# Performance work log

Measured on AMD Instinct MI355X. Metric: run time of the kernel, lower is better.

## Reference

```python
import jax, jax.numpy as jnp
import numpy as np

NHEADS = 16
DIM = 1024


def setup_inputs() -> dict:
    key = jax.random.key(0)
    k1, k2, k3 = jax.random.split(key, 3)
    B, S, D = 4, 2048, DIM
    x = jax.random.normal(k1, (B, S, D), dtype=jnp.float32)
    W_qkv = jax.random.normal(k2, (D, 3 * D), dtype=jnp.float32) * (1.0 / np.sqrt(D))
    b_qkv = jax.random.normal(k3, (3 * D,), dtype=jnp.float32) * 0.01
    return {"x": x, "W_qkv": W_qkv, "b_qkv": b_qkv}


def reference(x, W_qkv, b_qkv):
    B, S, D = x.shape
    H = NHEADS
    Dh = D // H
    qkv = x @ W_qkv + b_qkv                      # [B, S, 3D]
    q, k, v = jnp.split(qkv, 3, axis=-1)         # each [B, S, D]
    # [B, S, H, Dh] -> [B, H, S, Dh]
    q = q.reshape(B, S, H, Dh).transpose(0, 2, 1, 3)
    k = k.reshape(B, S, H, Dh).transpose(0, 2, 1, 3)
    v = v.reshape(B, S, H, Dh).transpose(0, 2, 1, 3)
    scale = 1.0 / np.sqrt(Dh).astype(np.float32)
    scores = jnp.einsum('bhqd,bhkd->bhqk', q, k) * scale
    attn = jax.nn.softmax(scores, axis=-1)
    out = jnp.einsum('bhqk,bhkd->bhqd', attn, v)  # [B, H, S, Dh]
    # FAITHFUL to original: raw view [B,H,S,Dh] -> [B, S, H*Dh] (no transpose back)
    return out.reshape(B, S, H * Dh)
```

## Files before the change

### kernel.cpp

```cpp
#include <hip/hip_runtime.h>
#include <hip/hip_bf16.h>
#include <stdint.h>

typedef float          f32x4 __attribute__((ext_vector_type(4)));
typedef short          s16x8 __attribute__((ext_vector_type(8)));
typedef unsigned short u16;
typedef u16            u16x4 __attribute__((ext_vector_type(4)));
typedef u16            u16x8 __attribute__((ext_vector_type(8)));

#define DMODEL 1024
#define NH     16
#define DH     64
#define SEQ    2048
#define BATCH  4
#define NROW   (BATCH*SEQ)
#define N3     (3*DMODEL)

#define KEXP 0.1803368801f

__device__ __forceinline__ u16 f2bf(float f) {
    __hip_bfloat16 h = __float2bfloat16(f);
    u16 u;
    __builtin_memcpy(&u, &h, 2);
    return u;
}

typedef const __attribute__((address_space(1))) void* gas_t;
typedef __attribute__((address_space(3))) void* las_t;
__device__ __forceinline__ void async16(void* lds, const void* g) {
    __builtin_amdgcn_global_load_lds((gas_t)g, (las_t)lds, 16, 0, 0);
}

__device__ __forceinline__ f32x4 mfma16(s16x8 a, s16x8 b, f32x4 c) {
    return __builtin_amdgcn_mfma_f32_16x16x32_bf16(a, b, c, 0, 0, 0);
}

__global__ __launch_bounds__(256)
void cast_x_kernel(const float* __restrict__ in, u16* __restrict__ out, int n8) {
    int i = blockIdx.x * 256 + threadIdx.x;
    if (i >= n8) return;
    const f32x4* p = (const f32x4*)in;
    f32x4 a = p[2*i], b = p[2*i+1];
    u16x8 o;
    o[0]=f2bf(a[0]); o[1]=f2bf(a[1]); o[2]=f2bf(a[2]); o[3]=f2bf(a[3]);
    o[4]=f2bf(b[0]); o[5]=f2bf(b[1]); o[6]=f2bf(b[2]); o[7]=f2bf(b[3]);
    ((u16x8*)out)[i] = o;
}

__global__ __launch_bounds__(256)
void castT_w_kernel(const float* __restrict__ W, u16* __restrict__ Wt) {
    __shared__ u16 T[64][72];
    const int t  = threadIdx.x;
    const int n0 = blockIdx.x * 64;
    const int k0 = blockIdx.y * 64;
    {
        const int c4 = t & 15, rr = t >> 4;
        #pragma unroll
        for (int ri = 0; ri < 4; ++ri) {
            const int r = ri*16 + rr;
            f32x4 v = *(const f32x4*)&W[(size_t)(k0 + r) * N3 + n0 + c4*4];
            #pragma unroll
            for (int e = 0; e < 4; ++e) T[r][c4*4+e] = f2bf(v[e]);
        }
    }
    __syncthreads();
    {
        const int nr = t >> 2, kq = t & 3;
        #pragma unroll
        for (int pp = 0; pp < 2; ++pp) {
            const int kb = kq + pp*4;
            u16x8 o;
            #pragma unroll
            for (int e = 0; e < 8; ++e) o[e] = T[kb*8+e][nr];
            *(u16x8*)&Wt[(size_t)(n0 + nr) * DMODEL + k0 + kb*8] = o;
        }
    }
}

__global__ __launch_bounds__(256)
void qkv_mfma_kernel(const u16* __restrict__ xb, const u16* __restrict__ Wt,
                     const float* __restrict__ bias,
                     u16* __restrict__ Qb, u16* __restrict__ Kb, u16* __restrict__ Vt)
{
    __shared__ u16 As[128*32];
    __shared__ u16 Bs[128*32];

    const int tid  = threadIdx.x;
    const int lane = tid & 63;
    const int w    = tid >> 6;
    const int wm   = w >> 1, wn = w & 1;
    const int n0   = blockIdx.x * 128;
    const int m0   = blockIdx.y * 128;

    const int srow = w*32 + (lane >> 2);
    const int scol = (lane & 3) * 8;
    u16* ad0 = &As[(w*2+0)*512 + lane*8];
    u16* ad1 = &As[(w*2+1)*512 + lane*8];
    u16* bd0 = &Bs[(w*2+0)*512 + lane*8];
    u16* bd1 = &Bs[(w*2+1)*512 + lane*8];
    const u16* ag0 = &xb[(size_t)(m0 + srow)      * DMODEL + scol];
    const u16* ag1 = &xb[(size_t)(m0 + srow + 16) * DMODEL + scol];
    const u16* bg0 = &Wt[(size_t)(n0 + srow)      * DMODEL + scol];
    const u16* bg1 = &Wt[(size_t)(n0 + srow + 16) * DMODEL + scol];

    f32x4 acc[4][4];
    #pragma unroll
    for (int i = 0; i < 4; ++i)
        #pragma unroll
        for (int j = 0; j < 4; ++j)
            acc[i][j] = (f32x4){0.f, 0.f, 0.f, 0.f};

    for (int k0 = 0; k0 < DMODEL; k0 += 32) {
        async16(ad0, ag0 + k0);
        async16(ad1, ag1 + k0);
        async16(bd0, bg0 + k0);
        async16(bd1, bg1 + k0);
        __syncthreads();
        s16x8 af[4], bf[4];
        #pragma unroll
        for (int mi = 0; mi < 4; ++mi)
            af[mi] = *(const s16x8*)&As[(wm*64 + mi*16 + (lane&15))*32 + (lane>>4)*8];
        #pragma unroll
        for (int ni = 0; ni < 4; ++ni)
            bf[ni] = *(const s16x8*)&Bs[(wn*64 + ni*16 + (lane&15))*32 + (lane>>4)*8];
        #pragma unroll
        for (int mi = 0; mi < 4; ++mi)
            #pragma unroll
            for (int ni = 0; ni < 4; ++ni)
                acc[mi][ni] = mfma16(af[mi], bf[ni], acc[mi][ni]);
        __syncthreads();
    }

    const int part  = n0 >> 10;
    const int col_l = lane & 15;
    const int h     = ((n0 & 1023) >> 6) + wn;
    float bv[4];
    #pragma unroll
    for (int ni = 0; ni < 4; ++ni) bv[ni] = bias[n0 + wn*64 + ni*16 + col_l];

    const int rbase = m0 + wm*64 + (lane>>4)*4;
    u16* qk = (part == 0) ? Qb : Kb;
    #pragma unroll
    for (int mi = 0; mi < 4; ++mi) {
        const int r0 = rbase + mi*16;
        const int b  = r0 >> 11;
        const int s  = r0 & 2047;
        #pragma unroll
        for (int ni = 0; ni < 4; ++ni) {
            const int d = ni*16 + col_l;
            if (part < 2) {
                u16* base = &qk[(((size_t)b*NH + h)*SEQ + s)*DH + d];
                #pragma unroll
                for (int j = 0; j < 4; ++j) {
                    float v = acc[mi][ni][j] + bv[ni];
                    if (part == 0) v *= KEXP;
                    base[(size_t)j*DH] = f2bf(v);
                }
            } else {
                u16x4 o;
                #pragma unroll
                for (int j = 0; j < 4; ++j) o[j] = f2bf(acc[mi][ni][j] + bv[ni]);
                *(u16x4*)&Vt[(((size_t)b*NH + h)*DH + d)*SEQ + s] = o;
            }
        }
    }
}

__global__ __launch_bounds__(512)
void attn_mfma_kernel(const u16* __restrict__ Qb, const u16* __restrict__ Kb,
                      const u16* __restrict__ Vt, float* __restrict__ out)
{
    __shared__ u16 Ks[2][64*64];
    __shared__ u16 Vs[2][64*64];
    __shared__ u16 Ps[8][32*64];

    const int tid  = threadIdx.x;
    const int lane = tid & 63;
    const int w    = tid >> 6;
    const int q0   = blockIdx.x * 256;
    const int bh   = blockIdx.y;
    const size_t qkoff = (size_t)bh * SEQ * DH;

    const int lrow = lane >> 4;
    const int lcol = lane & 15;

    s16x8 qf[2][2];
    #pragma unroll
    for (int mi = 0; mi < 2; ++mi) {
        const u16* qp = &Qb[qkoff + (size_t)(q0 + w*32 + mi*16 + lcol)*DH + lrow*8];
        qf[mi][0] = *(const s16x8*)(qp);
        qf[mi][1] = *(const s16x8*)(qp + 32);
    }

    const int skey = tid >> 3;
    const int sg   = tid & 7;
    const int gsw8 = (sg ^ (skey & 7)) * 8;
    const int sdo  = tid * 8;
    const u16* kgb = &Kb[qkoff + (size_t)skey * DH + gsw8];
    const u16* vgb = &Vt[((size_t)bh * DH + skey) * SEQ + gsw8];

    f32x4 oacc[2][4];
    #pragma unroll
    for (int mi = 0; mi < 2; ++mi)
        #pragma unroll
        for (int nd = 0; nd < 4; ++nd) oacc[mi][nd] = (f32x4){0.f,0.f,0.f,0.f};
    float psum[2][4];
    #pragma unroll
    for (int mi = 0; mi < 2; ++mi)
        #pragma unroll
        for (int j = 0; j < 4; ++j) psum[mi][j] = 0.f;

    u16* pw = Ps[w];

#define STAGE(buf, kb) do {                                       \
        const int _k0 = (kb) * 64;                                \
        async16(&Ks[buf][sdo], kgb + (size_t)_k0*DH);             \
        async16(&Vs[buf][sdo], vgb + _k0);                        \
    } while (0)

#define COMPUTE(buf) do {                                                        \
        const char* ksb = (const char*)Ks[buf];                                  \
        const char* vsb = (const char*)Vs[buf];                                  \
        f32x4 sacc[2][4];                                                        \
        _Pragma("unroll")                                                        \
        for (int mi = 0; mi < 2; ++mi)                                           \
            _Pragma("unroll")                                                    \
            for (int ni = 0; ni < 4; ++ni) sacc[mi][ni] = (f32x4){0.f,0.f,0.f,0.f}; \
        _Pragma("unroll")                                                        \
        for (int ni = 0; ni < 4; ++ni) {                                         \
            const int key  = ni*16 + lcol;                                       \
            const int rowb = key * 128;                                          \
            _Pragma("unroll")                                                    \
            for (int ks = 0; ks < 2; ++ks) {                                     \
                const int cb = (ks*64 + lrow*16) ^ ((key & 7) << 4);             \
                s16x8 kf = *(const s16x8*)(ksb + rowb + cb);                     \
                _Pragma("unroll")                                                \
                for (int mi = 0; mi < 2; ++mi)                                   \
                    sacc[mi][ni] = mfma16(qf[mi][ks], kf, sacc[mi][ni]);         \
            }                                                                    \
        }                                                                        \
        _Pragma("unroll")                                                        \
        for (int mi = 0; mi < 2; ++mi) {                                         \
            _Pragma("unroll")                                                    \
            for (int j = 0; j < 4; ++j) {                                        \
                const int q  = mi*16 + lrow*4 + j;                               \
                const int sw = ((q & 7) << 4);                                   \
                float rs = 0.f;                                                  \
                _Pragma("unroll")                                                \
                for (int ni = 0; ni < 4; ++ni) {                                 \
                    const float p = __builtin_amdgcn_exp2f(sacc[mi][ni][j]);     \
                    rs += p;                                                     \
                    const int key = ni*16 + lcol;                                \
                    *(u16*)((char*)pw + q*128 + ((key*2) ^ sw)) = f2bf(p);       \
                }                                                                \
                psum[mi][j] += rs;                                               \
            }                                                                    \
        }                                                                        \
        _Pragma("unroll")                                                        \
        for (int ks = 0; ks < 2; ++ks) {                                         \
            const int psw = ((lcol & 7) << 4);                                   \
            s16x8 pa[2];                                                         \
            _Pragma("unroll")                                                    \
            for (int mi = 0; mi < 2; ++mi)                                       \
                pa[mi] = *(const s16x8*)((const char*)pw + (mi*16 + lcol)*128    \
                                         + ((ks*64 + lrow*16) ^ psw));           \
            _Pragma("unroll")                                                    \
            for (int nd = 0; nd < 4; ++nd) {                                     \
                const int d  = nd*16 + lcol;                                     \
                const int vb = d*128 + ((ks*64 + lrow*16) ^ ((d & 7) << 4));     \
                s16x8 vf = *(const s16x8*)(vsb + vb);                            \
                _Pragma("unroll")                                                \
                for (int mi = 0; mi < 2; ++mi)                                   \
                    oacc[mi][nd] = mfma16(pa[mi], vf, oacc[mi][nd]);             \
            }                                                                    \
        }                                                                        \
    } while (0)

    STAGE(0, 0);
    asm volatile("s_waitcnt vmcnt(0)" ::: "memory");
    __builtin_amdgcn_s_barrier();

    for (int kb = 0; kb < SEQ/64; kb += 2) {
        STAGE(1, kb + 1);
        COMPUTE(0);
        asm volatile("s_waitcnt vmcnt(0)" ::: "memory");
        __builtin_amdgcn_s_barrier();
        if (kb + 2 < SEQ/64) STAGE(0, kb + 2);
        COMPUTE(1);
        asm volatile("s_waitcnt vmcnt(0)" ::: "memory");
        __builtin_amdgcn_s_barrier();
    }

#undef STAGE
#undef COMPUTE

    float* op = out + qkoff;
    #pragma unroll
    for (int mi = 0; mi < 2; ++mi) {
        #pragma unroll
        for (int j = 0; j < 4; ++j) {
            float l = psum[mi][j];
            l += __shfl_xor(l, 1);
            l += __shfl_xor(l, 2);
            l += __shfl_xor(l, 4);
            l += __shfl_xor(l, 8);
            const float rinv = 1.0f / l;
            const int q = q0 + w*32 + mi*16 + lrow*4 + j;
            #pragma unroll
            for (int nd = 0; nd < 4; ++nd)
                op[(size_t)q*DH + nd*16 + lcol] = oacc[mi][nd][j] * rinv;
        }
    }
}

extern "C" void kernel_launch(void* const* d_in, const int* in_sizes, int n_in,
                              void* d_out, int out_size, void* d_ws, size_t ws_size,
                              hipStream_t stream)
{
    const float* x    = (const float*)d_in[0];
    const float* W    = (const float*)d_in[1];
    const float* bias = (const float*)d_in[2];
    float* out = (float*)d_out;

    u16* xb = (u16*)d_ws;
    u16* Wt = xb + (size_t)NROW * DMODEL;
    u16* Qb = Wt + (size_t)N3 * DMODEL;
    u16* Kb = Qb + (size_t)BATCH*NH*SEQ*DH;
    u16* Vt = Kb + (size_t)BATCH*NH*SEQ*DH;

    cast_x_kernel<<<4096, 256, 0, stream>>>(x, xb, NROW*DMODEL/8);
    castT_w_kernel<<<dim3(N3/64, DMODEL/64), 256, 0, stream>>>(W, Wt);
    qkv_mfma_kernel<<<dim3(N3/128, NROW/128), 256, 0, stream>>>(xb, Wt, bias, Qb, Kb, Vt);
    attn_mfma_kernel<<<dim3(SEQ/256, BATCH*NH), 512, 0, stream>>>(Qb, Kb, Vt, out);
}
```

Baseline: 184.1 us.

## Keep softmax probabilities in registers via transposed QK^T and K=16 MFMA

Swaps the operand order of the QK^T MFMA so each lane holds scores for consecutive keys of one query. The exponentiated probabilities can then feed a 16x16x16 bf16 MFMA for P·V straight from registers, removing the per-wave LDS round trip for P and its shared buffer. The row-sum reduction becomes a cross-lane shuffle over lanes 16/32, with a shuffle broadcast at the end. The trade-off is twice as many smaller-K MFMAs for P·V and narrower 8-byte V reads from LDS.

```diff
diff --git a/kernel.cpp b/kernel.cpp
--- a/kernel.cpp
+++ b/kernel.cpp
@@ -4,6 +4,7 @@
 
 typedef float          f32x4 __attribute__((ext_vector_type(4)));
 typedef short          s16x8 __attribute__((ext_vector_type(8)));
+typedef short          s16x4 __attribute__((ext_vector_type(4)));
 typedef unsigned short u16;
 typedef u16            u16x4 __attribute__((ext_vector_type(4)));
 typedef u16            u16x8 __attribute__((ext_vector_type(8)));
@@ -34,6 +35,22 @@
 __device__ __forceinline__ f32x4 mfma16(s16x8 a, s16x8 b, f32x4 c) {
     return __builtin_amdgcn_mfma_f32_16x16x32_bf16(a, b, c, 0, 0, 0);
 }
+
+#if !defined(__HIP_DEVICE_COMPILE__)
+__device__ __forceinline__ f32x4 mfma16k16(s16x4 a, s16x4 b, f32x4 c) {
+    (void)a; (void)b; return c;
+}
+#elif __has_builtin(__builtin_amdgcn_mfma_f32_16x16x16bf16_1k)
+__device__ __forceinline__ f32x4 mfma16k16(s16x4 a, s16x4 b, f32x4 c) {
+    return __builtin_amdgcn_mfma_f32_16x16x16bf16_1k(a, b, c, 0, 0, 0);
+}
+#elif __has_builtin(__builtin_amdgcn_mfma_f32_16x16x16_bf16)
+__device__ __forceinline__ f32x4 mfma16k16(s16x4 a, s16x4 b, f32x4 c) {
+    return __builtin_amdgcn_mfma_f32_16x16x16_bf16(a, b, c, 0, 0, 0);
+}
+#else
+#error "no 16x16x16 bf16 mfma builtin on device"
+#endif
 
 __global__ __launch_bounds__(256)
 void cast_x_kernel(const float* __restrict__ in, u16* __restrict__ out, int n8) {
@@ -172,7 +189,6 @@
 {
     __shared__ u16 Ks[2][64*64];
     __shared__ u16 Vs[2][64*64];
-    __shared__ u16 Ps[8][32*64];
 
     const int tid  = threadIdx.x;
     const int lane = tid & 63;
@@ -204,13 +220,7 @@
     for (int mi = 0; mi < 2; ++mi)
         #pragma unroll
         for (int nd = 0; nd < 4; ++nd) oacc[mi][nd] = (f32x4){0.f,0.f,0.f,0.f};
-    float psum[2][4];
-    #pragma unroll
-    for (int mi = 0; mi < 2; ++mi)
-        #pragma unroll
-        for (int j = 0; j < 4; ++j) psum[mi][j] = 0.f;
-
-    u16* pw = Ps[w];
+    float psum[2] = {0.f, 0.f};
 
 #define STAGE(buf, kb) do {                                       \
         const int _k0 = (kb) * 64;                                \
@@ -236,42 +246,39 @@
                 s16x8 kf = *(const s16x8*)(ksb + rowb + cb);                     \
                 _Pragma("unroll")                                                \
                 for (int mi = 0; mi < 2; ++mi)                                   \
-                    sacc[mi][ni] = mfma16(qf[mi][ks], kf, sacc[mi][ni]);         \
+                    sacc[mi][ni] = mfma16(kf, qf[mi][ks], sacc[mi][ni]);         \
             }                                                                    \
         }                                                                        \
+                \
+        s16x4 pa[2][4];                                                          \
         _Pragma("unroll")                                                        \
         for (int mi = 0; mi < 2; ++mi) {                                         \
+            float rs = 0.f;                                                      \
             _Pragma("unroll")                                                    \
-            for (int j = 0; j < 4; ++j) {                                        \
-                const int q  = mi*16 + lrow*4 + j;                               \
-                const int sw = ((q & 7) << 4);                                   \
-                float rs = 0.f;                                                  \
+            for (int ni = 0; ni < 4; ++ni) {                                     \
+                u16x4 pk;                                                        \
                 _Pragma("unroll")                                                \
-                for (int ni = 0; ni < 4; ++ni) {                                 \
-                    const float p = __builtin_amdgcn_exp2f(sacc[mi][ni][j]);     \
+                for (int jj = 0; jj < 4; ++jj) {                                 \
+                    const float p = __builtin_amdgcn_exp2f(sacc[mi][ni][jj]);    \
                     rs += p;                                                     \
-                    const int key = ni*16 + lcol;                                \
-                    *(u16*)((char*)pw + q*128 + ((key*2) ^ sw)) = f2bf(p);       \
+                    pk[jj] = f2bf(p);                                            \
                 }                                                                \
-                psum[mi][j] += rs;                                               \
+                pa[mi][ni] = (s16x4)pk;                                          \
             }                                                                    \
+            psum[mi] += rs;                                                      \
         }                                                                        \
+                \
         _Pragma("unroll")                                                        \
-        for (int ks = 0; ks < 2; ++ks) {                                         \
-            const int psw = ((lcol & 7) << 4);                                   \
-            s16x8 pa[2];                                                         \
-            _Pragma("unroll")                                                    \
-            for (int mi = 0; mi < 2; ++mi)                                       \
-                pa[mi] = *(const s16x8*)((const char*)pw + (mi*16 + lcol)*128    \
-                                         + ((ks*64 + lrow*16) ^ psw));           \
+        for (int ni = 0; ni < 4; ++ni) {                                         \
             _Pragma("unroll")                                                    \
             for (int nd = 0; nd < 4; ++nd) {                                     \
-                const int d  = nd*16 + lcol;                                     \
-                const int vb = d*128 + ((ks*64 + lrow*16) ^ ((d & 7) << 4));     \
-                s16x8 vf = *(const s16x8*)(vsb + vb);                            \
+                const int d    = nd*16 + lcol;                                   \
+                const int gran = ni*2 + (lrow >> 1);                             \
+                const int vb   = d*128 + ((gran ^ (d & 7)) << 4) + (lrow & 1)*8; \
+                s16x4 vf = *(const s16x4*)(vsb + vb);                            \
                 _Pragma("unroll")                                                \
                 for (int mi = 0; mi < 2; ++mi)                                   \
-                    oacc[mi][nd] = mfma16(pa[mi], vf, oacc[mi][nd]);             \
+                    oacc[mi][nd] = mfma16k16(pa[mi][ni], vf, oacc[mi][nd]);      \
             }                                                                    \
         }                                                                        \
     } while (0)
@@ -297,18 +304,16 @@
     float* op = out + qkoff;
     #pragma unroll
     for (int mi = 0; mi < 2; ++mi) {
-        #pragma unroll
-        for (int j = 0; j < 4; ++j) {
-            float l = psum[mi][j];
-            l += __shfl_xor(l, 1);
-            l += __shfl_xor(l, 2);
-            l += __shfl_xor(l, 4);
-            l += __shfl_xor(l, 8);
-            const float rinv = 1.0f / l;
-            const int q = q0 + w*32 + mi*16 + lrow*4 + j;
+        float l = psum[mi];
+        l += __shfl_xor(l, 16);
+        l += __shfl_xor(l, 32);
+        #pragma unroll
+        for (int jj = 0; jj < 4; ++jj) {
+            const float rinv = 1.0f / __shfl(l, lrow*4 + jj);
+            const int q = q0 + w*32 + mi*16 + lrow*4 + jj;
             #pragma unroll
             for (int nd = 0; nd < 4; ++nd)
-                op[(size_t)q*DH + nd*16 + lcol] = oacc[mi][nd][j] * rinv;
+                op[(size_t)q*DH + nd*16 + lcol] = oacc[mi][nd][jj] * rinv;
         }
     }
 }
```

Result: no change. 182.3 us (-1.0%).
